# Kernel optimization log

Hardware: AMD Instinct MI355X
Metric: run time of the kernel (lower is better)

## Reference

```python
import jax, jax.numpy as jnp
import numpy as np

N_NODES = 50000
N_EDGES = 800000
IN_CH = 128
HEADS = 4
OUT_CH = 32


def setup_inputs() -> dict:
    key = jax.random.key(0)
    k1, k2, k3, k4 = jax.random.split(key, 4)
    x = jax.random.normal(k1, (N_NODES, IN_CH), dtype=jnp.float32)
    edge_index = jax.random.randint(k2, (2, N_EDGES), 0, N_NODES, dtype=jnp.int64)
    # nn.Linear weight [out, in] with xavier-uniform init
    limW = float(np.sqrt(6.0 / (IN_CH + HEADS * OUT_CH)))
    W = jax.random.uniform(k3, (HEADS * OUT_CH, IN_CH), minval=-limW, maxval=limW, dtype=jnp.float32)
    lima = float(np.sqrt(6.0 / (HEADS + 2 * OUT_CH)))
    att = jax.random.uniform(k4, (HEADS, 2 * OUT_CH), minval=-lima, maxval=lima, dtype=jnp.float32)
    bias = jnp.zeros((HEADS * OUT_CH,), dtype=jnp.float32)
    return {"x": x, "edge_index": edge_index, "W": W, "att": att, "bias": bias}


def reference(x, edge_index, W, att, bias):
    n = x.shape[0]
    heads, two_c = att.shape
    out_ch = two_c // 2
    loop = jnp.arange(n, dtype=edge_index.dtype)
    src = jnp.concatenate([edge_index[0], loop])  # [E+n]
    dst = jnp.concatenate([edge_index[1], loop])  # [E+n]
    h = (x @ W.T).reshape(n, heads, out_ch)       # [n, H, C]
    h_src = h[src]                                # [E+n, H, C]
    h_dst = h[dst]                                # [E+n, H, C]
    # e = sum over channels of att applied to [h_src || h_dst]
    e = (jnp.einsum('ehc,hc->eh', h_src, att[:, :out_ch])
         + jnp.einsum('ehc,hc->eh', h_dst, att[:, out_ch:]))  # [E+n, H]
    e = jax.nn.leaky_relu(e, negative_slope=0.2)
    # segment softmax over incoming edges per dst node
    e_max = jax.ops.segment_max(e, dst, num_segments=n)        # [n, H]
    alpha = jnp.exp(e - e_max[dst])                            # [E+n, H]
    a_sum = jax.ops.segment_sum(alpha, dst, num_segments=n)    # [n, H]
    alpha = alpha / jnp.maximum(a_sum[dst], 1e-10)
    weighted = h_src * alpha[..., None]                        # [E+n, H, C]
    out = jax.ops.segment_sum(weighted, dst, num_segments=n)   # [n, H, C]
    out = out.reshape(n, heads * out_ch)                       # concat=True
    return out + bias
```

## Files before the change

### kernel.cpp

```cpp
#include <hip/hip_runtime.h>
#include <hip/hip_bf16.h>
#include <math.h>

#define N_NODES 50000
#define N_EDGES 800000
#define IN_CH   128
#define HEADS   4
#define OUT_CH  32
#define HC      128
#define WROWS   136

#define CB_SHIFT 7
#define CB_NODES 128
#define N_CB     391
#define NBK      128
#define EPB      (N_EDGES / NBK)
#define PCAP     44
#define ND_CAP   48

#define NG_TOT   782
#define S_SUB    4

typedef __attribute__((ext_vector_type(8))) short short8;
typedef __attribute__((ext_vector_type(4))) float floatx4;

__device__ __forceinline__ short f2bf(float f) {
    __hip_bfloat16 h = __float2bfloat16(f);
    return *reinterpret_cast<short*>(&h);
}

__device__ __forceinline__ void gemm_role(
    short* __restrict__ Wlds, int node_base,
    const float* __restrict__ x, const float* __restrict__ W,
    const float* __restrict__ att, __hip_bfloat16* __restrict__ hbuf,
    float* __restrict__ asrc, float* __restrict__ adst) {

    const int tid  = threadIdx.x;
    const int wave = tid >> 6;
    const int lane = tid & 63;
    const int col  = lane & 15;
    const int q    = lane >> 4;

    {
        int row  = tid >> 1;
        int half = tid & 1;
        const float4* Wr = (const float4*)(W + row * IN_CH + half * 64);
        short* dp = Wlds + row * WROWS + half * 64;
#pragma unroll
        for (int i = 0; i < 16; ++i) {
            float4 v = Wr[i];
            ushort4 p;
            p.x = (unsigned short)f2bf(v.x);
            p.y = (unsigned short)f2bf(v.y);
            p.z = (unsigned short)f2bf(v.z);
            p.w = (unsigned short)f2bf(v.w);
            *(ushort4*)(dp + i * 4) = p;
        }
    }

    float attS[8], attD[8];
#pragma unroll
    for (int t = 0; t < 8; ++t) {
        int base = (t >> 1) * 64 + (t & 1) * 16 + col;
        attS[t] = att[base];
        attD[t] = att[base + 32];
    }

    __syncthreads();

    const int node0 = node_base + wave * 16;
    const int m  = node0 + col;
    const int mc = min(m, N_NODES - 1);

    floatx4 acc[8];
#pragma unroll
    for (int t = 0; t < 8; ++t) acc[t] = (floatx4){0.f, 0.f, 0.f, 0.f};

#pragma unroll
    for (int ks = 0; ks < 4; ++ks) {
        const float4* xp = (const float4*)(x + (size_t)mc * IN_CH + ks * 32 + q * 8);
        float4 v0 = xp[0];
        float4 v1 = xp[1];
        short8 af;
        af[0] = f2bf(v0.x); af[1] = f2bf(v0.y); af[2] = f2bf(v0.z); af[3] = f2bf(v0.w);
        af[4] = f2bf(v1.x); af[5] = f2bf(v1.y); af[6] = f2bf(v1.z); af[7] = f2bf(v1.w);
#pragma unroll
        for (int t = 0; t < 8; ++t) {
            const short8 bf = *(const short8*)(Wlds + (t * 16 + col) * WROWS + ks * 32 + q * 8);
            acc[t] = __builtin_amdgcn_mfma_f32_16x16x32_bf16(af, bf, acc[t], 0, 0, 0);
        }
    }

#pragma unroll
    for (int r = 0; r < 4; ++r) {
        const int node = node0 + q * 4 + r;
        const bool valid = node < N_NODES;
        float hs[4] = {0.f, 0.f, 0.f, 0.f};
        float hd[4] = {0.f, 0.f, 0.f, 0.f};
#pragma unroll
        for (int t = 0; t < 8; ++t) {
            float v = acc[t][r];
            if (valid) hbuf[(size_t)node * HC + t * 16 + col] = __float2bfloat16(v);
            hs[t >> 1] = fmaf(v, attS[t], hs[t >> 1]);
            hd[t >> 1] = fmaf(v, attD[t], hd[t >> 1]);
        }
#pragma unroll
        for (int off = 8; off; off >>= 1) {
#pragma unroll
            for (int h = 0; h < 4; ++h) {
                hs[h] += __shfl_down(hs[h], off, 16);
                hd[h] += __shfl_down(hd[h], off, 16);
            }
        }
        if (col == 0 && valid) {
#pragma unroll
            for (int h = 0; h < 4; ++h) {
                asrc[node * HEADS + h] = hs[h];
                adst[node * HEADS + h] = hd[h];
            }
        }
    }
}

__global__ __launch_bounds__(256) void k1_fused(
    const int* __restrict__ src, const int* __restrict__ dst,
    unsigned* __restrict__ priv, int* __restrict__ cnt2t,
    const float* __restrict__ x, const float* __restrict__ W,
    const float* __restrict__ att, __hip_bfloat16* __restrict__ hbuf,
    float* __restrict__ asrc, float* __restrict__ adst) {

    __shared__ short smem[128 * WROWS];
    const int tid = threadIdx.x;

    if (blockIdx.x < NBK) {
        int* lcnt = (int*)smem;
        const int blk = blockIdx.x;
        for (int i = tid; i < N_CB; i += 256) lcnt[i] = 0;
        __syncthreads();

        const int e0 = blk * EPB;
        for (int e = e0 + tid; e < e0 + EPB; e += 256) {
            int s = src[e];
            int d = dst[e];
            int cb = d >> CB_SHIFT;
            int pos = atomicAdd(&lcnt[cb], 1);
            if (pos < PCAP)
                priv[((size_t)cb * NBK + blk) * PCAP + pos] =
                    ((unsigned)(d & (CB_NODES - 1)) << 16) | (unsigned)s;
        }
        __syncthreads();
        for (int i = tid; i < N_CB; i += 256)
            cnt2t[i * NBK + blk] = min(lcnt[i], PCAP);
        return;
    }

    gemm_role(smem, (blockIdx.x - NBK) * 64, x, W, att, hbuf, asrc, adst);
}

__device__ __forceinline__ float edge_w(float t) {
    t = fmaxf(t, 0.2f * t);
    return __expf(t);
}

__device__ __forceinline__ void agg_one(
    int node, int cnt, const unsigned short* __restrict__ p,
    const unsigned* __restrict__ hb, const float* __restrict__ asrc,
    const float* __restrict__ adst, const float* __restrict__ bias,
    float* __restrict__ out, int lane, int h) {

    const float ad = adst[node * HEADS + h];

    unsigned us = hb[node * 64 + lane];
    float wS = edge_w(asrc[node * HEADS + h] + ad);
    float ds = wS;
    float ax = wS * __uint_as_float(us << 16);
    float ay = wS * __uint_as_float(us & 0xffff0000u);

    int e = 0;
    for (; e + 7 < cnt; e += 8) {
        int s0 = p[e],     s1 = p[e + 1], s2 = p[e + 2], s3 = p[e + 3];
        int s4 = p[e + 4], s5 = p[e + 5], s6 = p[e + 6], s7 = p[e + 7];
        unsigned u0 = hb[s0 * 64 + lane];
        unsigned u1 = hb[s1 * 64 + lane];
        unsigned u2 = hb[s2 * 64 + lane];
        unsigned u3 = hb[s3 * 64 + lane];
        unsigned u4 = hb[s4 * 64 + lane];
        unsigned u5 = hb[s5 * 64 + lane];
        unsigned u6 = hb[s6 * 64 + lane];
        unsigned u7 = hb[s7 * 64 + lane];
        float w0 = edge_w(asrc[s0 * HEADS + h] + ad);
        float w1 = edge_w(asrc[s1 * HEADS + h] + ad);
        float w2 = edge_w(asrc[s2 * HEADS + h] + ad);
        float w3 = edge_w(asrc[s3 * HEADS + h] + ad);
        float w4 = edge_w(asrc[s4 * HEADS + h] + ad);
        float w5 = edge_w(asrc[s5 * HEADS + h] + ad);
        float w6 = edge_w(asrc[s6 * HEADS + h] + ad);
        float w7 = edge_w(asrc[s7 * HEADS + h] + ad);
        ds += ((w0 + w1) + (w2 + w3)) + ((w4 + w5) + (w6 + w7));
        ax = fmaf(w0, __uint_as_float(u0 << 16), ax);
        ay = fmaf(w0, __uint_as_float(u0 & 0xffff0000u), ay);
        ax = fmaf(w1, __uint_as_float(u1 << 16), ax);
        ay = fmaf(w1, __uint_as_float(u1 & 0xffff0000u), ay);
        ax = fmaf(w2, __uint_as_float(u2 << 16), ax);
        ay = fmaf(w2, __uint_as_float(u2 & 0xffff0000u), ay);
        ax = fmaf(w3, __uint_as_float(u3 << 16), ax);
        ay = fmaf(w3, __uint_as_float(u3 & 0xffff0000u), ay);
        ax = fmaf(w4, __uint_as_float(u4 << 16), ax);
        ay = fmaf(w4, __uint_as_float(u4 & 0xffff0000u), ay);
        ax = fmaf(w5, __uint_as_float(u5 << 16), ax);
        ay = fmaf(w5, __uint_as_float(u5 & 0xffff0000u), ay);
        ax = fmaf(w6, __uint_as_float(u6 << 16), ax);
        ay = fmaf(w6, __uint_as_float(u6 & 0xffff0000u), ay);
        ax = fmaf(w7, __uint_as_float(u7 << 16), ax);
        ay = fmaf(w7, __uint_as_float(u7 & 0xffff0000u), ay);
    }
    for (; e + 3 < cnt; e += 4) {
        int s0 = p[e], s1 = p[e + 1], s2 = p[e + 2], s3 = p[e + 3];
        unsigned u0 = hb[s0 * 64 + lane];
        unsigned u1 = hb[s1 * 64 + lane];
        unsigned u2 = hb[s2 * 64 + lane];
        unsigned u3 = hb[s3 * 64 + lane];
        float w0 = edge_w(asrc[s0 * HEADS + h] + ad);
        float w1 = edge_w(asrc[s1 * HEADS + h] + ad);
        float w2 = edge_w(asrc[s2 * HEADS + h] + ad);
        float w3 = edge_w(asrc[s3 * HEADS + h] + ad);
        ds += (w0 + w1) + (w2 + w3);
        ax = fmaf(w0, __uint_as_float(u0 << 16), ax);
        ay = fmaf(w0, __uint_as_float(u0 & 0xffff0000u), ay);
        ax = fmaf(w1, __uint_as_float(u1 << 16), ax);
        ay = fmaf(w1, __uint_as_float(u1 & 0xffff0000u), ay);
        ax = fmaf(w2, __uint_as_float(u2 << 16), ax);
        ay = fmaf(w2, __uint_as_float(u2 & 0xffff0000u), ay);
        ax = fmaf(w3, __uint_as_float(u3 << 16), ax);
        ay = fmaf(w3, __uint_as_float(u3 & 0xffff0000u), ay);
    }
    for (; e < cnt; ++e) {
        int s0 = p[e];
        unsigned u0 = hb[s0 * 64 + lane];
        float w0 = edge_w(asrc[s0 * HEADS + h] + ad);
        ds += w0;
        ax = fmaf(w0, __uint_as_float(u0 << 16), ax);
        ay = fmaf(w0, __uint_as_float(u0 & 0xffff0000u), ay);
    }

    float inv = 1.0f / fmaxf(ds, 1e-10f);
    float2 b = *(const float2*)(bias + lane * 2);
    float2 o;
    o.x = ax * inv + b.x;
    o.y = ay * inv + b.y;
    *(float2*)(out + (size_t)node * HC + lane * 2) = o;
}

__global__ __launch_bounds__(256) void k2_binagg(
    const int* __restrict__ cnt2t, const unsigned* __restrict__ priv,
    const unsigned* __restrict__ hb, const float* __restrict__ asrc,
    const float* __restrict__ adst, const float* __restrict__ bias,
    float* __restrict__ out) {

    __shared__ unsigned short list[32 * ND_CAP];
    __shared__ int lcnt[32];
    __shared__ int lcnt2[NBK];

    const int b   = blockIdx.x >> 2;
    const int sub = blockIdx.x & (S_SUB - 1);
    const int tid = threadIdx.x;

    if (tid < 32) lcnt[tid] = 0;
    if (tid < NBK) lcnt2[tid] = cnt2t[b * NBK + tid];
    __syncthreads();

    const unsigned* p = priv + (size_t)b * (NBK * PCAP);
    for (int idx = tid; idx < NBK * PCAP; idx += 256) {
        int blk = (idx * 5958) >> 18;
        int j   = idx - blk * PCAP;
        if (j < lcnt2[blk]) {
            unsigned ent = p[idx];
            int dl = ent >> 16;
            if ((dl >> 5) == sub) {
                int slot = atomicAdd(&lcnt[dl & 31], 1);
                if (slot < ND_CAP)
                    list[(dl & 31) * ND_CAP + slot] = (unsigned short)(ent & 0xFFFFu);
            }
        }
    }
    __syncthreads();

    const int wv   = tid >> 6;
    const int lane = tid & 63;
    const int h    = lane >> 4;

#pragma unroll 1
    for (int rr = 0; rr < 8; ++rr) {
        const int dl   = (sub << 5) + (wv << 3) + rr;
        const int node = (b << CB_SHIFT) + dl;
        if (node >= N_NODES) break;
        const int cnt = min(lcnt[dl & 31], ND_CAP);
        agg_one(node, cnt, &list[(dl & 31) * ND_CAP],
                hb, asrc, adst, bias, out, lane, h);
    }
}

extern "C" void kernel_launch(void* const* d_in, const int* in_sizes, int n_in,
                              void* d_out, int out_size, void* d_ws, size_t ws_size,
                              hipStream_t stream) {
    const float* x    = (const float*)d_in[0];
    const int*   ei   = (const int*)d_in[1];
    const float* W    = (const float*)d_in[2];
    const float* att  = (const float*)d_in[3];
    const float* bias = (const float*)d_in[4];
    float* out = (float*)d_out;

    const int* src = ei;
    const int* dst = ei + N_EDGES;

    char* ws = (char*)d_ws;
    __hip_bfloat16* hbuf = (__hip_bfloat16*)ws;
    float*    asrc = (float*)(ws + 12800000);
    float*    adst = (float*)(ws + 13600000);
    unsigned* priv = (unsigned*)(ws + 14400000);
    int*      cnt2 = (int*)(ws + 23208448);

    k1_fused<<<NBK + NG_TOT, 256, 0, stream>>>(src, dst, priv, cnt2,
                                               x, W, att, hbuf, asrc, adst);
    k2_binagg<<<N_CB * S_SUB, 256, 0, stream>>>(cnt2, priv, (const unsigned*)hbuf,
                                                asrc, adst, bias, out);
}
```

Before: 150.0 us.

## Halve destination bucket size and scan each bucket once with 1024-thread blocks

```diff
diff --git a/kernel.cpp b/kernel.cpp
--- a/kernel.cpp
+++ b/kernel.cpp
@@ -10,18 +10,18 @@
 #define HC      128
 #define WROWS   136
 
-#define CB_SHIFT 7
-#define CB_NODES 128
-#define N_CB     391
+#define CB_SHIFT 6
+#define CB_NODES 64
+#define N_CB     782
 #define NBK      128
 #define EPB      (N_EDGES / NBK)
-#define PCAP     44
+#define PCAP     28
 #define ND_CAP   48
 
 #define NG_TOT   782
-#define S_SUB    4
 
 typedef __attribute__((ext_vector_type(8))) short short8;
+typedef __attribute__((ext_vector_type(8))) unsigned short ushort8;
 typedef __attribute__((ext_vector_type(4))) float floatx4;
 
 __device__ __forceinline__ short f2bf(float f) {
@@ -165,7 +165,7 @@
 __device__ __forceinline__ void agg_one(
     int node, int cnt, const unsigned short* __restrict__ p,
     const unsigned* __restrict__ hb, const float* __restrict__ asrc,
-    const float* __restrict__ adst, const float* __restrict__ bias,
+    const float* __restrict__ adst, float2 bv,
     float* __restrict__ out, int lane, int h) {
 
     const float ad = adst[node * HEADS + h];
@@ -178,8 +178,9 @@
 
     int e = 0;
     for (; e + 7 < cnt; e += 8) {
-        int s0 = p[e],     s1 = p[e + 1], s2 = p[e + 2], s3 = p[e + 3];
-        int s4 = p[e + 4], s5 = p[e + 5], s6 = p[e + 6], s7 = p[e + 7];
+        ushort8 sv = *(const ushort8*)(p + e);
+        int s0 = sv[0], s1 = sv[1], s2 = sv[2], s3 = sv[3];
+        int s4 = sv[4], s5 = sv[5], s6 = sv[6], s7 = sv[7];
         unsigned u0 = hb[s0 * 64 + lane];
         unsigned u1 = hb[s1 * 64 + lane];
         unsigned u2 = hb[s2 * 64 + lane];
@@ -244,43 +245,39 @@
     }
 
     float inv = 1.0f / fmaxf(ds, 1e-10f);
-    float2 b = *(const float2*)(bias + lane * 2);
     float2 o;
-    o.x = ax * inv + b.x;
-    o.y = ay * inv + b.y;
+    o.x = ax * inv + bv.x;
+    o.y = ay * inv + bv.y;
     *(float2*)(out + (size_t)node * HC + lane * 2) = o;
 }
 
-__global__ __launch_bounds__(256) void k2_binagg(
+__global__ __launch_bounds__(1024) void k2_binagg(
     const int* __restrict__ cnt2t, const unsigned* __restrict__ priv,
     const unsigned* __restrict__ hb, const float* __restrict__ asrc,
     const float* __restrict__ adst, const float* __restrict__ bias,
     float* __restrict__ out) {
 
-    __shared__ unsigned short list[32 * ND_CAP];
-    __shared__ int lcnt[32];
+    __shared__ unsigned short list[CB_NODES * ND_CAP];
+    __shared__ int lcnt[CB_NODES];
     __shared__ int lcnt2[NBK];
 
-    const int b   = blockIdx.x >> 2;
-    const int sub = blockIdx.x & (S_SUB - 1);
+    const int b   = blockIdx.x;
     const int tid = threadIdx.x;
 
-    if (tid < 32) lcnt[tid] = 0;
+    if (tid < CB_NODES) lcnt[tid] = 0;
     if (tid < NBK) lcnt2[tid] = cnt2t[b * NBK + tid];
     __syncthreads();
 
     const unsigned* p = priv + (size_t)b * (NBK * PCAP);
-    for (int idx = tid; idx < NBK * PCAP; idx += 256) {
-        int blk = (idx * 5958) >> 18;
+    for (int idx = tid; idx < NBK * PCAP; idx += 1024) {
+        int blk = (idx * 4682) >> 17;
         int j   = idx - blk * PCAP;
         if (j < lcnt2[blk]) {
             unsigned ent = p[idx];
-            int dl = ent >> 16;
-            if ((dl >> 5) == sub) {
-                int slot = atomicAdd(&lcnt[dl & 31], 1);
-                if (slot < ND_CAP)
-                    list[(dl & 31) * ND_CAP + slot] = (unsigned short)(ent & 0xFFFFu);
-            }
+            int dl   = ent >> 16;
+            int slot = atomicAdd(&lcnt[dl], 1);
+            if (slot < ND_CAP)
+                list[dl * ND_CAP + slot] = (unsigned short)(ent & 0xFFFFu);
         }
     }
     __syncthreads();
@@ -288,15 +285,16 @@
     const int wv   = tid >> 6;
     const int lane = tid & 63;
     const int h    = lane >> 4;
+    const float2 bv = *(const float2*)(bias + lane * 2);
 
 #pragma unroll 1
-    for (int rr = 0; rr < 8; ++rr) {
-        const int dl   = (sub << 5) + (wv << 3) + rr;
+    for (int rr = 0; rr < 4; ++rr) {
+        const int dl   = (wv << 2) + rr;
         const int node = (b << CB_SHIFT) + dl;
         if (node >= N_NODES) break;
-        const int cnt = min(lcnt[dl & 31], ND_CAP);
-        agg_one(node, cnt, &list[(dl & 31) * ND_CAP],
-                hb, asrc, adst, bias, out, lane, h);
+        const int cnt = min(lcnt[dl], ND_CAP);
+        agg_one(node, cnt, &list[dl * ND_CAP],
+                hb, asrc, adst, bv, out, lane, h);
     }
 }
 
@@ -318,10 +316,10 @@
     float*    asrc = (float*)(ws + 12800000);
     float*    adst = (float*)(ws + 13600000);
     unsigned* priv = (unsigned*)(ws + 14400000);
-    int*      cnt2 = (int*)(ws + 23208448);
+    int*      cnt2 = (int*)(ws + 25610752);
 
     k1_fused<<<NBK + NG_TOT, 256, 0, stream>>>(src, dst, priv, cnt2,
                                                x, W, att, hbuf, asrc, adst);
-    k2_binagg<<<N_CB * S_SUB, 256, 0, stream>>>(cnt2, priv, (const unsigned*)hbuf,
-                                                asrc, adst, bias, out);
-}
+    k2_binagg<<<N_CB, 1024, 0, stream>>>(cnt2, priv, (const unsigned*)hbuf,
+                                         asrc, adst, bias, out);
+}
```

Result: no change. 149.2 us (-0.6%).
